# Kernel tuning notes

Measured on AMD Instinct MI355X. Metric: run time of the kernel, lower is better.

## Reference

```python
import jax, jax.numpy as jnp
import numpy as np

# Semantics of GPTQ Marlin 2:4 int4 GEMM: W_dense[K,N] has exactly 2 nonzeros per
# group of 4 along K. Compressed int4 values (q-8)*scale are stored packed 8-per-int32
# in B [K/16, N]; meta [K/4, N] in [0,6) selects which pair of the 4 positions is
# nonzero (index into the 6 combinations). s [K/groupsize, N] are group scales.

_PAIRS = jnp.array([[0, 1], [0, 2], [0, 3], [1, 2], [1, 3], [2, 3]], dtype=jnp.int32)


def _dequant_24(B, meta, s):
    Kd16, N = B.shape
    K = Kd16 * 16
    # unpack 8 nibbles per int32 -> [K/2, N] compressed values
    shifts = (jnp.arange(8, dtype=jnp.int32) * 4)[None, :, None]
    nib = (B[:, None, :] >> shifts) & 0xF            # [K/16, 8, N]
    vals = nib.reshape(K // 2, N).astype(jnp.float32) - 8.0  # symmetric zero-point 8
    gs = K // s.shape[0]                              # original groupsize
    scale = jnp.repeat(s, gs // 2, axis=0)            # [K/2, N] (compressed K dim)
    deq = (vals * scale).reshape(K // 4, 2, N)        # 2 values per group of 4
    pos = _PAIRS[meta]                                # [K/4, N, 2] positions in [0,4)
    oh = jax.nn.one_hot(pos, 4, dtype=jnp.float32)    # [K/4, N, 2, 4]
    W = jnp.einsum('gjn,gnjp->gpn', deq, oh)          # scatter into group slots
    return W.reshape(K, N)


def setup_inputs() -> dict:
    key = jax.random.key(0)
    k0, k1, k2, k3, k4 = jax.random.split(key, 5)
    M, K, N, GS = 8192, 4096, 4096, 128
    A = jax.random.normal(k0, (M, K), dtype=jnp.float32)
    B = jax.random.randint(k1, (K // 16, N), 0, 2147483647, dtype=jnp.int32)
    meta = jax.random.randint(k2, (K // 4, N), 0, 6, dtype=jnp.int32)
    s = jax.random.uniform(k3, (K // GS, N), dtype=jnp.float32, minval=0.005, maxval=0.02)
    bias = jax.random.normal(k4, (N,), dtype=jnp.float32)
    return {"A": A, "B": B, "meta": meta, "s": s, "bias": bias}


def reference(A, B, meta, s, bias):
    W = _dequant_24(B, meta, s)          # [K, N] dense 2:4-sparse dequantized weight
    return jnp.matmul(A, W, preferred_element_type=jnp.float32) + bias
```

## Files before the change

### kernel.cpp

```cpp
#include <hip/hip_runtime.h>

typedef _Float16 h16;
typedef __attribute__((ext_vector_type(8))) _Float16 h16x8;
typedef __attribute__((ext_vector_type(4))) float f32x4;
typedef unsigned int u32;

#define BARRIER() __builtin_amdgcn_s_barrier()
#define SCHEDB()  __builtin_amdgcn_sched_barrier(0)

__global__ __launch_bounds__(256) void cvtA_kernel(const float* __restrict__ A,
                                                   h16* __restrict__ Ah, int total8) {
  int stride = gridDim.x * blockDim.x;
  for (int i = blockIdx.x * blockDim.x + threadIdx.x; i < total8; i += stride) {
    const f32x4* p = (const f32x4*)(A + (size_t)i * 8);
    f32x4 v0 = p[0], v1 = p[1];
    h16x8 o;
    o[0] = (h16)v0[0]; o[1] = (h16)v0[1]; o[2] = (h16)v0[2]; o[3] = (h16)v0[3];
    o[4] = (h16)v1[0]; o[5] = (h16)v1[1]; o[6] = (h16)v1[2]; o[7] = (h16)v1[3];
    *(h16x8*)(Ah + (size_t)i * 8) = o;
  }
}

__global__ __launch_bounds__(256) void dequant_kernel(const int* __restrict__ Bq,
    const int* __restrict__ meta, const float* __restrict__ s,
    h16* __restrict__ Wt, int K, int N, int chunksPerGroup) {
  int n = blockIdx.x * 256 + threadIdx.x;
  int chunk = blockIdx.y;
  u32 w0 = (u32)Bq[(size_t)(chunk * 2) * N + n];
  u32 w1 = (u32)Bq[(size_t)(chunk * 2 + 1) * N + n];
  float sc = s[(size_t)(chunk / chunksPerGroup) * N + n];
  h16 out[32];
#pragma unroll
  for (int gi = 0; gi < 8; ++gi) {
    int g = chunk * 8 + gi;
    int mm = meta[(size_t)g * N + n];
    u32 w = (gi < 4) ? w0 : w1;
    int j0 = (2 * gi) & 7;
    float d0 = (float)((int)((w >> (4 * j0)) & 0xFu) - 8) * sc;
    float d1 = (float)((int)((w >> (4 * j0 + 4)) & 0xFu) - 8) * sc;
    u32 enc = (0xED9C84u >> (4 * mm)) & 0xFu;
    int p0 = (int)(enc & 3u), p1 = (int)(enc >> 2);
#pragma unroll
    for (int p = 0; p < 4; ++p) {
      float v = (p == p0) ? d0 : ((p == p1) ? d1 : 0.0f);
      out[gi * 4 + p] = (h16)v;
    }
  }
  h16* dst = Wt + (size_t)n * K + chunk * 32;
  *(h16x8*)(dst + 0)  = *(h16x8*)(out + 0);
  *(h16x8*)(dst + 8)  = *(h16x8*)(out + 8);
  *(h16x8*)(dst + 16) = *(h16x8*)(out + 16);
  *(h16x8*)(dst + 24) = *(h16x8*)(out + 24);
}

__global__ __launch_bounds__(512, 2) void gemm_kernel(const h16* __restrict__ A,
    const h16* __restrict__ Wt, const float* __restrict__ bias,
    float* __restrict__ C, int M, int N, int K) {
  __shared__ alignas(16) h16 As[2 * 2 * 8192];
  __shared__ alignas(16) h16 Bs[2 * 2 * 8192];

  const int nTilesN = N >> 8;
  const int nwg = gridDim.x;
  int bid = blockIdx.x;
  int wg = (bid & 7) * (nwg >> 3) + (bid >> 3);
  int tm = wg / nTilesN, tn = wg - tm * nTilesN;

  const int tid = threadIdx.x;
  const int lane = tid & 63, w = tid >> 6;
  const int wr = w >> 2, wc = w & 3;

  const int i0 = tid >> 3;
  const int sigma = (tid & 7) ^ ((tid >> 3) & 7);
  const h16* gA_t = A + ((size_t)(tm * 256) + i0) * K + sigma * 8;
  const int rB0 = ((i0 >> 5) << 6) + (i0 & 31);
  const h16* gB_t = Wt + ((size_t)(tn * 256) + rB0) * K + sigma * 8;
  const int tid8 = tid * 8;
  const size_t rowK128 = (size_t)128 * K;

#define GLOAD(SRC, DST) __builtin_amdgcn_global_load_lds(                      \
    (const __attribute__((address_space(1))) void*)(SRC),                      \
    (__attribute__((address_space(3))) void*)(DST), 16, 0, 0)

#define STAGE_A(T_, mh_) do {                                                  \
    const h16* s_ = gA_t + (size_t)((mh_) * 64) * K + (T_) * 64;               \
    h16* d_ = As + ((((T_) & 1) * 2 + (mh_)) * 8192) + tid8;                   \
    GLOAD(s_, d_); GLOAD(s_ + rowK128, d_ + 4096); } while (0)

#define STAGE_B(T_, nh_) do {                                                  \
    const h16* s_ = gB_t + (size_t)((nh_) * 32) * K + (T_) * 64;               \
    h16* d_ = Bs + ((((T_) & 1) * 2 + (nh_)) * 8192) + tid8;                   \
    GLOAD(s_, d_); GLOAD(s_ + rowK128, d_ + 4096); } while (0)

  const int ln15 = lane & 15, l16 = lane >> 4, l7 = lane & 7;
  const int aRow = (wr * 64 + ln15) * 64;
  const int bRow = (wc * 32 + ln15) * 64;
  const int sl0 = ((0 + l16) ^ l7) * 8;
  const int sl1 = ((4 + l16) ^ l7) * 8;

  f32x4 acc[8][4] = {};
  const int NT = K >> 6;

  STAGE_A(0, 0); STAGE_B(0, 0); STAGE_B(0, 1); STAGE_A(0, 1);
  STAGE_A(1, 0); STAGE_B(1, 0); STAGE_B(1, 1);
  asm volatile("s_waitcnt vmcnt(6)" ::: "memory");
  SCHEDB();
  BARRIER();
  SCHEDB();

  for (int T = 0; T < NT; ++T) {
    const int buf = T & 1;
    const h16* a0 = As + (buf * 2 + 0) * 8192;
    const h16* a1 = As + (buf * 2 + 1) * 8192;
    const h16* b0 = Bs + (buf * 2 + 0) * 8192;
    const h16* b1 = Bs + (buf * 2 + 1) * 8192;
    h16x8 af[4][2], bf0[2][2], bf1[2][2];

#pragma unroll
    for (int m = 0; m < 4; ++m) {
      af[m][0] = *(const h16x8*)(a0 + aRow + m * 1024 + sl0);
      af[m][1] = *(const h16x8*)(a0 + aRow + m * 1024 + sl1);
    }
#pragma unroll
    for (int n = 0; n < 2; ++n) {
      bf0[n][0] = *(const h16x8*)(b0 + bRow + n * 1024 + sl0);
      bf0[n][1] = *(const h16x8*)(b0 + bRow + n * 1024 + sl1);
    }
    if (T + 1 < NT) STAGE_A(T + 1, 1);
    asm volatile("s_waitcnt lgkmcnt(8)" ::: "memory");
    SCHEDB();
    BARRIER();
    asm volatile("s_waitcnt lgkmcnt(0)" ::: "memory");
    SCHEDB();
    __builtin_amdgcn_s_setprio(1);
#pragma unroll
    for (int m = 0; m < 4; ++m)
#pragma unroll
      for (int n = 0; n < 2; ++n) {
        acc[m][n] = __builtin_amdgcn_mfma_f32_16x16x32_f16(af[m][0], bf0[n][0], acc[m][n], 0, 0, 0);
        acc[m][n] = __builtin_amdgcn_mfma_f32_16x16x32_f16(af[m][1], bf0[n][1], acc[m][n], 0, 0, 0);
      }
    __builtin_amdgcn_s_setprio(0);
    SCHEDB();
    BARRIER();

#pragma unroll
    for (int n = 0; n < 2; ++n) {
      bf1[n][0] = *(const h16x8*)(b1 + bRow + n * 1024 + sl0);
      bf1[n][1] = *(const h16x8*)(b1 + bRow + n * 1024 + sl1);
    }
    if (T + 2 < NT) STAGE_A(T + 2, 0);
    SCHEDB();
    BARRIER();
    asm volatile("s_waitcnt lgkmcnt(0)" ::: "memory");
    SCHEDB();
    __builtin_amdgcn_s_setprio(1);
#pragma unroll
    for (int m = 0; m < 4; ++m)
#pragma unroll
      for (int n = 0; n < 2; ++n) {
        acc[m][2 + n] = __builtin_amdgcn_mfma_f32_16x16x32_f16(af[m][0], bf1[n][0], acc[m][2 + n], 0, 0, 0);
        acc[m][2 + n] = __builtin_amdgcn_mfma_f32_16x16x32_f16(af[m][1], bf1[n][1], acc[m][2 + n], 0, 0, 0);
      }
    __builtin_amdgcn_s_setprio(0);
    SCHEDB();
    BARRIER();

#pragma unroll
    for (int m = 0; m < 4; ++m) {
      af[m][0] = *(const h16x8*)(a1 + aRow + m * 1024 + sl0);
      af[m][1] = *(const h16x8*)(a1 + aRow + m * 1024 + sl1);
    }
    if (T + 2 < NT) STAGE_B(T + 2, 0);
    SCHEDB();
    BARRIER();
    asm volatile("s_waitcnt lgkmcnt(0)" ::: "memory");
    SCHEDB();
    __builtin_amdgcn_s_setprio(1);
#pragma unroll
    for (int m = 0; m < 4; ++m)
#pragma unroll
      for (int n = 0; n < 2; ++n) {
        acc[4 + m][2 + n] = __builtin_amdgcn_mfma_f32_16x16x32_f16(af[m][0], bf1[n][0], acc[4 + m][2 + n], 0, 0, 0);
        acc[4 + m][2 + n] = __builtin_amdgcn_mfma_f32_16x16x32_f16(af[m][1], bf1[n][1], acc[4 + m][2 + n], 0, 0, 0);
      }
    __builtin_amdgcn_s_setprio(0);
    SCHEDB();
    BARRIER();

    if (T + 2 < NT) STAGE_B(T + 2, 1);
    SCHEDB();
    BARRIER();
    SCHEDB();
    __builtin_amdgcn_s_setprio(1);
#pragma unroll
    for (int m = 0; m < 4; ++m)
#pragma unroll
      for (int n = 0; n < 2; ++n) {
        acc[4 + m][n] = __builtin_amdgcn_mfma_f32_16x16x32_f16(af[m][0], bf0[n][0], acc[4 + m][n], 0, 0, 0);
        acc[4 + m][n] = __builtin_amdgcn_mfma_f32_16x16x32_f16(af[m][1], bf0[n][1], acc[4 + m][n], 0, 0, 0);
      }
    __builtin_amdgcn_s_setprio(0);
    SCHEDB();
    if (T < NT - 2) {
      asm volatile("s_waitcnt vmcnt(6)" ::: "memory");
    } else if (T == NT - 2) {
      asm volatile("s_waitcnt vmcnt(0)" ::: "memory");
    }
    SCHEDB();
    BARRIER();
    SCHEDB();
  }

  int colBase = tn * 256 + wc * 64 + ln15;
  int rowBase = tm * 256 + wr * 128 + l16 * 4;
#pragma unroll
  for (int n = 0; n < 4; ++n) {
    float bv = bias[colBase + n * 16];
#pragma unroll
    for (int m = 0; m < 8; ++m) {
#pragma unroll
      for (int j = 0; j < 4; ++j) {
        C[(size_t)(rowBase + m * 16 + j) * N + colBase + n * 16] = acc[m][n][j] + bv;
      }
    }
  }
#undef STAGE_A
#undef STAGE_B
#undef GLOAD
}

extern "C" void kernel_launch(void* const* d_in, const int* in_sizes, int n_in,
                              void* d_out, int out_size, void* d_ws, size_t ws_size,
                              hipStream_t stream) {
  const float* A = (const float*)d_in[0];
  const int* Bq = (const int*)d_in[1];
  const int* meta = (const int*)d_in[2];
  const float* s = (const float*)d_in[3];
  const float* bias = (const float*)d_in[4];
  float* C = (float*)d_out;

  const int N = in_sizes[4];
  const int K = (int)(((long long)in_sizes[1] * 16) / N);
  const int M = (int)((long long)in_sizes[0] / K);
  const int sRows = (int)((long long)in_sizes[3] / N);
  const int chunksPerGroup = (K / sRows) / 32;

  h16* Ah = (h16*)d_ws;
  h16* Wt = Ah + (size_t)M * K;

  cvtA_kernel<<<2048, 256, 0, stream>>>(A, Ah, (M * K) / 8);

  dim3 dgrid(N / 256, K / 32);
  dequant_kernel<<<dgrid, 256, 0, stream>>>(Bq, meta, s, Wt, K, N, chunksPerGroup);

  int grid = (M / 256) * (N / 256);
  gemm_kernel<<<grid, 512, 0, stream>>>(Ah, Wt, bias, C, M, N, K);
}
```

Measured before the change: 295.0 us.

## Switch GEMM inner loop from 16x16x32 to 32x32x16 MFMA tiles

Replaces the 16x16x32 f16 MFMA tiling with 32x32x16 MFMA instructions. Each wave now keeps a 4x2 grid of 32x32 accumulators, and the LDS fragment indexing and epilogue store mapping are rewritten to match the 32-lane row layout. The larger MFMA does more work per issued instruction and needs fewer LDS fragment reads per FLOP. In exchange it changes LDS access patterns and register pressure. A few sched_barriers around the barriers are also removed.

```diff
diff --git a/kernel.cpp b/kernel.cpp
--- a/kernel.cpp
+++ b/kernel.cpp
@@ -3,6 +3,7 @@
 typedef _Float16 h16;
 typedef __attribute__((ext_vector_type(8))) _Float16 h16x8;
 typedef __attribute__((ext_vector_type(4))) float f32x4;
+typedef __attribute__((ext_vector_type(16))) float f32x16;
 typedef unsigned int u32;
 
 #define BARRIER() __builtin_amdgcn_s_barrier()
@@ -91,13 +92,14 @@
     h16* d_ = Bs + ((((T_) & 1) * 2 + (nh_)) * 8192) + tid8;                   \
     GLOAD(s_, d_); GLOAD(s_ + rowK128, d_ + 4096); } while (0)
 
-  const int ln15 = lane & 15, l16 = lane >> 4, l7 = lane & 7;
-  const int aRow = (wr * 64 + ln15) * 64;
-  const int bRow = (wc * 32 + ln15) * 64;
-  const int sl0 = ((0 + l16) ^ l7) * 8;
-  const int sl1 = ((4 + l16) ^ l7) * 8;
-
-  f32x4 acc[8][4] = {};
+  const int l31 = lane & 31, l5 = lane >> 5, l7 = lane & 7;
+  const int aR = (wr * 64 + l31) * 64;
+  const int bR = (wc * 32 + l31) * 64;
+  int sl[4];
+#pragma unroll
+  for (int kst = 0; kst < 4; ++kst) sl[kst] = ((kst * 2 + l5) ^ l7) * 8;
+
+  f32x16 acc[4][2] = {};
   const int NT = K >> 6;
 
   STAGE_A(0, 0); STAGE_B(0, 0); STAGE_B(0, 1); STAGE_A(0, 1);
@@ -105,7 +107,6 @@
   asm volatile("s_waitcnt vmcnt(6)" ::: "memory");
   SCHEDB();
   BARRIER();
-  SCHEDB();
 
   for (int T = 0; T < NT; ++T) {
     const int buf = T & 1;
@@ -113,18 +114,15 @@
     const h16* a1 = As + (buf * 2 + 1) * 8192;
     const h16* b0 = Bs + (buf * 2 + 0) * 8192;
     const h16* b1 = Bs + (buf * 2 + 1) * 8192;
-    h16x8 af[4][2], bf0[2][2], bf1[2][2];
-
-#pragma unroll
-    for (int m = 0; m < 4; ++m) {
-      af[m][0] = *(const h16x8*)(a0 + aRow + m * 1024 + sl0);
-      af[m][1] = *(const h16x8*)(a0 + aRow + m * 1024 + sl1);
-    }
-#pragma unroll
-    for (int n = 0; n < 2; ++n) {
-      bf0[n][0] = *(const h16x8*)(b0 + bRow + n * 1024 + sl0);
-      bf0[n][1] = *(const h16x8*)(b0 + bRow + n * 1024 + sl1);
-    }
+    h16x8 af[2][4], bf0[4], bf1[4];
+
+#pragma unroll
+    for (int k = 0; k < 4; ++k) bf0[k] = *(const h16x8*)(b0 + bR + sl[k]);
+#pragma unroll
+    for (int mtl = 0; mtl < 2; ++mtl)
+#pragma unroll
+      for (int k = 0; k < 4; ++k)
+        af[mtl][k] = *(const h16x8*)(a0 + aR + mtl * 2048 + sl[k]);
     if (T + 1 < NT) STAGE_A(T + 1, 1);
     asm volatile("s_waitcnt lgkmcnt(8)" ::: "memory");
     SCHEDB();
@@ -133,21 +131,16 @@
     SCHEDB();
     __builtin_amdgcn_s_setprio(1);
 #pragma unroll
-    for (int m = 0; m < 4; ++m)
-#pragma unroll
-      for (int n = 0; n < 2; ++n) {
-        acc[m][n] = __builtin_amdgcn_mfma_f32_16x16x32_f16(af[m][0], bf0[n][0], acc[m][n], 0, 0, 0);
-        acc[m][n] = __builtin_amdgcn_mfma_f32_16x16x32_f16(af[m][1], bf0[n][1], acc[m][n], 0, 0, 0);
-      }
-    __builtin_amdgcn_s_setprio(0);
-    SCHEDB();
-    BARRIER();
-
-#pragma unroll
-    for (int n = 0; n < 2; ++n) {
-      bf1[n][0] = *(const h16x8*)(b1 + bRow + n * 1024 + sl0);
-      bf1[n][1] = *(const h16x8*)(b1 + bRow + n * 1024 + sl1);
-    }
+    for (int k = 0; k < 4; ++k)
+#pragma unroll
+      for (int mtl = 0; mtl < 2; ++mtl)
+        acc[mtl][0] = __builtin_amdgcn_mfma_f32_32x32x16_f16(af[mtl][k], bf0[k], acc[mtl][0], 0, 0, 0);
+    __builtin_amdgcn_s_setprio(0);
+    SCHEDB();
+    BARRIER();
+
+#pragma unroll
+    for (int k = 0; k < 4; ++k) bf1[k] = *(const h16x8*)(b1 + bR + sl[k]);
     if (T + 2 < NT) STAGE_A(T + 2, 0);
     SCHEDB();
     BARRIER();
@@ -155,21 +148,19 @@
     SCHEDB();
     __builtin_amdgcn_s_setprio(1);
 #pragma unroll
-    for (int m = 0; m < 4; ++m)
-#pragma unroll
-      for (int n = 0; n < 2; ++n) {
-        acc[m][2 + n] = __builtin_amdgcn_mfma_f32_16x16x32_f16(af[m][0], bf1[n][0], acc[m][2 + n], 0, 0, 0);
-        acc[m][2 + n] = __builtin_amdgcn_mfma_f32_16x16x32_f16(af[m][1], bf1[n][1], acc[m][2 + n], 0, 0, 0);
-      }
-    __builtin_amdgcn_s_setprio(0);
-    SCHEDB();
-    BARRIER();
-
-#pragma unroll
-    for (int m = 0; m < 4; ++m) {
-      af[m][0] = *(const h16x8*)(a1 + aRow + m * 1024 + sl0);
-      af[m][1] = *(const h16x8*)(a1 + aRow + m * 1024 + sl1);
-    }
+    for (int k = 0; k < 4; ++k)
+#pragma unroll
+      for (int mtl = 0; mtl < 2; ++mtl)
+        acc[mtl][1] = __builtin_amdgcn_mfma_f32_32x32x16_f16(af[mtl][k], bf1[k], acc[mtl][1], 0, 0, 0);
+    __builtin_amdgcn_s_setprio(0);
+    SCHEDB();
+    BARRIER();
+
+#pragma unroll
+    for (int mtl = 0; mtl < 2; ++mtl)
+#pragma unroll
+      for (int k = 0; k < 4; ++k)
+        af[mtl][k] = *(const h16x8*)(a1 + aR + mtl * 2048 + sl[k]);
     if (T + 2 < NT) STAGE_B(T + 2, 0);
     SCHEDB();
     BARRIER();
@@ -177,12 +168,10 @@
     SCHEDB();
     __builtin_amdgcn_s_setprio(1);
 #pragma unroll
-    for (int m = 0; m < 4; ++m)
-#pragma unroll
-      for (int n = 0; n < 2; ++n) {
-        acc[4 + m][2 + n] = __builtin_amdgcn_mfma_f32_16x16x32_f16(af[m][0], bf1[n][0], acc[4 + m][2 + n], 0, 0, 0);
-        acc[4 + m][2 + n] = __builtin_amdgcn_mfma_f32_16x16x32_f16(af[m][1], bf1[n][1], acc[4 + m][2 + n], 0, 0, 0);
-      }
+    for (int k = 0; k < 4; ++k)
+#pragma unroll
+      for (int mtl = 0; mtl < 2; ++mtl)
+        acc[2 + mtl][1] = __builtin_amdgcn_mfma_f32_32x32x16_f16(af[mtl][k], bf1[k], acc[2 + mtl][1], 0, 0, 0);
     __builtin_amdgcn_s_setprio(0);
     SCHEDB();
     BARRIER();
@@ -193,14 +182,11 @@
     SCHEDB();
     __builtin_amdgcn_s_setprio(1);
 #pragma unroll
-    for (int m = 0; m < 4; ++m)
-#pragma unroll
-      for (int n = 0; n < 2; ++n) {
-        acc[4 + m][n] = __builtin_amdgcn_mfma_f32_16x16x32_f16(af[m][0], bf0[n][0], acc[4 + m][n], 0, 0, 0);
-        acc[4 + m][n] = __builtin_amdgcn_mfma_f32_16x16x32_f16(af[m][1], bf0[n][1], acc[4 + m][n], 0, 0, 0);
-      }
-    __builtin_amdgcn_s_setprio(0);
-    SCHEDB();
+    for (int k = 0; k < 4; ++k)
+#pragma unroll
+      for (int mtl = 0; mtl < 2; ++mtl)
+        acc[2 + mtl][0] = __builtin_amdgcn_mfma_f32_32x32x16_f16(af[mtl][k], bf0[k], acc[2 + mtl][0], 0, 0, 0);
+    __builtin_amdgcn_s_setprio(0);
     if (T < NT - 2) {
       asm volatile("s_waitcnt vmcnt(6)" ::: "memory");
     } else if (T == NT - 2) {
@@ -208,19 +194,22 @@
     }
     SCHEDB();
     BARRIER();
-    SCHEDB();
-  }
-
-  int colBase = tn * 256 + wc * 64 + ln15;
-  int rowBase = tm * 256 + wr * 128 + l16 * 4;
-#pragma unroll
-  for (int n = 0; n < 4; ++n) {
-    float bv = bias[colBase + n * 16];
-#pragma unroll
-    for (int m = 0; m < 8; ++m) {
-#pragma unroll
-      for (int j = 0; j < 4; ++j) {
-        C[(size_t)(rowBase + m * 16 + j) * N + colBase + n * 16] = acc[m][n][j] + bv;
+  }
+
+  int colB = tn * 256 + wc * 64 + l31;
+  int rowB = tm * 256 + wr * 128 + l5 * 4;
+#pragma unroll
+  for (int nt = 0; nt < 2; ++nt) {
+    float bv = bias[colB + nt * 32];
+#pragma unroll
+    for (int mt = 0; mt < 4; ++mt) {
+#pragma unroll
+      for (int q = 0; q < 4; ++q) {
+#pragma unroll
+        for (int j = 0; j < 4; ++j) {
+          C[(size_t)(rowB + mt * 32 + q * 8 + j) * N + colB + nt * 32] =
+              acc[mt][nt][q * 4 + j] + bv;
+        }
       }
     }
   }
```

New measurement: 320.5 us. 1.09x slower.
